# Performance work log

Hardware: AMD Instinct MI355X
Metric: run time of the kernel (lower is better)

Reference implementation:

```python
import jax, jax.numpy as jnp
import numpy as np

EMBED_DIM = 1024
NUM_HEADS = 16
HEAD_DIM = EMBED_DIM // NUM_HEADS
SCALE = float(np.sqrt(HEAD_DIM))


def setup_inputs() -> dict:
    key = jax.random.key(0)
    ks = jax.random.split(key, 5)
    B, S, D = 4, 2048, EMBED_DIM
    lim_qkv = 1.0 / np.sqrt(D)
    lim_out = 1.0 / np.sqrt(D)
    return {
        "x": jax.random.normal(ks[0], (B, S, D), dtype=jnp.float32),
        "qkv_w": jax.random.uniform(ks[1], (3 * D, D), jnp.float32, -lim_qkv, lim_qkv),
        "qkv_b": jax.random.uniform(ks[2], (3 * D,), jnp.float32, -lim_qkv, lim_qkv),
        "out_w": jax.random.uniform(ks[3], (D, D), jnp.float32, -lim_out, lim_out),
        "out_b": jax.random.uniform(ks[4], (D,), jnp.float32, -lim_out, lim_out),
    }


def reference(x, qkv_w, qkv_b, out_w, out_b):
    B, S, D = x.shape
    H, Hd = NUM_HEADS, HEAD_DIM
    # qkv projection (torch Linear: x @ W.T + b)
    qkv = x @ qkv_w.T + qkv_b                      # [B, S, 3D]
    qkv = qkv.reshape(B, S, 3, H, Hd)
    q = jnp.transpose(qkv[:, :, 0], (0, 2, 1, 3))  # [B, H, S, Hd]
    k = jnp.transpose(qkv[:, :, 1], (0, 2, 1, 3))
    v = jnp.transpose(qkv[:, :, 2], (0, 2, 1, 3))
    attn = jnp.einsum("bhqd,bhkd->bhqk", q, k) / SCALE  # [B, H, S, S]
    attn = jax.nn.softmax(attn, axis=-1)
    out = jnp.einsum("bhqk,bhkd->bhqd", attn, v)        # [B, H, S, Hd]
    out = jnp.transpose(out, (0, 2, 1, 3)).reshape(B, S, D)
    return out @ out_w.T + out_b
```

## Files before the change

### kernel.cpp

```cpp
#include <hip/hip_runtime.h>

typedef unsigned short u16;
typedef __bf16 bf16x8 __attribute__((ext_vector_type(8)));
typedef __bf16 bf16x4 __attribute__((ext_vector_type(4)));
typedef float f32x4 __attribute__((ext_vector_type(4)));
typedef float f32x16 __attribute__((ext_vector_type(16)));
typedef unsigned u32x2 __attribute__((ext_vector_type(2)));

#define AS1 __attribute__((address_space(1)))
#define AS3 __attribute__((address_space(3)))

__device__ __forceinline__ void gload_lds16(const void* g, void* l) {
  __builtin_amdgcn_global_load_lds((const AS1 void*)g, (AS3 void*)l, 16, 0, 0);
}

__device__ __forceinline__ f32x4 mfma16(bf16x8 a, bf16x8 b, f32x4 c) {
  return __builtin_amdgcn_mfma_f32_16x16x32_bf16(a, b, c, 0, 0, 0);
}
__device__ __forceinline__ f32x16 mfma32(bf16x8 a, bf16x8 b, f32x16 c) {
  return __builtin_amdgcn_mfma_f32_32x32x16_bf16(a, b, c, 0, 0, 0);
}

#define QSCALE 0.18033688011112042f

__global__ __launch_bounds__(256) void k_cvt3(const float* __restrict__ s0, u16* __restrict__ d0, int n0,
                                              const float* __restrict__ s1, u16* __restrict__ d1, int n1,
                                              const float* __restrict__ s2, u16* __restrict__ d2, int n2) {
  int g = (blockIdx.x * 256 + threadIdx.x) * 8;
  const float* src;
  u16* dst;
  int i;
  if (g < n0) { src = s0; dst = d0; i = g; }
  else if (g < n0 + n1) { src = s1; dst = d1; i = g - n0; }
  else if (g < n0 + n1 + n2) { src = s2; dst = d2; i = g - n0 - n1; }
  else return;
  float4 a = *(const float4*)(src + i);
  float4 b = *(const float4*)(src + i + 4);
  union { bf16x8 v; uint4 q; } o;
  o.v[0] = (__bf16)a.x; o.v[1] = (__bf16)a.y; o.v[2] = (__bf16)a.z; o.v[3] = (__bf16)a.w;
  o.v[4] = (__bf16)b.x; o.v[5] = (__bf16)b.y; o.v[6] = (__bf16)b.z; o.v[7] = (__bf16)b.w;
  *(uint4*)(dst + i) = o.q;
}

__global__ __launch_bounds__(512, 2) void k_gemm_qkv(
    const u16* __restrict__ A, const u16* __restrict__ W,
    const float* __restrict__ bias,
    u16* __restrict__ Qo, u16* __restrict__ Ko, u16* __restrict__ Vo) {
  __shared__ __align__(16) u16 LDS[2][6 * 4096];

  const int t = threadIdx.x;
  const int lane = t & 63;
  const int w = t >> 6;
  const int wm = w >> 1;
  const int wn = w & 1;
  const int lr = lane & 15;
  const int hi = lane >> 4;

  const int flat = blockIdx.x;
  const int nb = (flat & 7) * 96 + (flat >> 3);
  const int by = nb / 24;
  const int bx = nb - by * 24;
  const int m0 = by * 256;
  const int n0 = bx * 128;

  const int tt = t & 255;
  const int g = t >> 8;
  const int tu = (tt & 15) ^ (tt >> 4);
  const int sro = (tu >> 3) * 32 + (tt >> 4);
  const int scol = (tu & 7) * 8;

  auto STAGE = [&](int buf, int kt) {
#pragma unroll
    for (int p = 0; p < 3; ++p) {
      int st = p * 2 + g;
      const u16* base = (st < 4) ? (A + (size_t)(m0 + st * 64) * 1024)
                                 : (W + (size_t)(n0 + (st - 4) * 64) * 1024);
#pragma unroll
      for (int i = 0; i < 2; ++i)
        gload_lds16(base + (size_t)(sro + i * 16) * 1024 + kt * 64 + scol,
                    &LDS[buf][st * 4096 + i * 2048 + tt * 8]);
    }
  };

  f32x4 acc[4][4] = {};

  STAGE(0, 0);

  for (int kt = 0; kt < 16; ++kt) {
    const int cur = kt & 1;
    asm volatile("s_waitcnt vmcnt(0)" ::: "memory");
    __builtin_amdgcn_sched_barrier(0);
    __builtin_amdgcn_s_barrier();
    __builtin_amdgcn_sched_barrier(0);

    if (kt + 1 < 16) STAGE(cur ^ 1, kt + 1);

    const u16* ab = &LDS[cur][wm * 4096];
    const u16* bb = &LDS[cur][(4 + wn) * 4096];

    bf16x8 af[4][2], bfr[4][2];
#pragma unroll
    for (int mi = 0; mi < 4; ++mi)
#pragma unroll
      for (int ks = 0; ks < 2; ++ks)
        af[mi][ks] = *(const bf16x8*)(ab + ((mi & 1) * 16 + lr) * 128 +
                                      (((ks * 4 + hi + 8 * (mi >> 1)) ^ lr) << 3));
#pragma unroll
    for (int ni = 0; ni < 4; ++ni)
#pragma unroll
      for (int ks = 0; ks < 2; ++ks)
        bfr[ni][ks] = *(const bf16x8*)(bb + ((ni & 1) * 16 + lr) * 128 +
                                       (((ks * 4 + hi + 8 * (ni >> 1)) ^ lr) << 3));

    __builtin_amdgcn_s_setprio(1);
#pragma unroll
    for (int mi = 0; mi < 4; ++mi)
#pragma unroll
      for (int ni = 0; ni < 4; ++ni)
#pragma unroll
        for (int ks = 0; ks < 2; ++ks)
          acc[mi][ni] = mfma16(bfr[ni][ks], af[mi][ks], acc[mi][ni]);
    __builtin_amdgcn_s_setprio(0);
  }

  const int bb16 = m0 >> 11;
  const int sb = (m0 & 2047) + wm * 64;
  const int which = n0 >> 10;
  const int h = ((n0 & 1023) >> 6) + wn;
  float4 bv[4];
#pragma unroll
  for (int ni = 0; ni < 4; ++ni)
    bv[ni] = *(const float4*)(bias + n0 + wn * 64 + ni * 16 + hi * 4);

  if (which < 2) {
    const float scl = (which == 0) ? QSCALE : 1.0f;
    u16* dst = ((which == 0) ? Qo : Ko) + ((size_t)(bb16 * 16 + h) * 2048) * 64;
#pragma unroll
    for (int mi = 0; mi < 4; ++mi) {
      const int s = sb + mi * 16 + lr;
#pragma unroll
      for (int ni = 0; ni < 4; ++ni) {
        bf16x4 pk;
#pragma unroll
        for (int j = 0; j < 4; ++j)
          pk[j] = (__bf16)((acc[mi][ni][j] + ((const float*)&bv[ni])[j]) * scl);
        *(bf16x4*)(dst + (size_t)s * 64 + ni * 16 + hi * 4) = pk;
      }
    }
  } else {
    __syncthreads();
    u16* scr = &LDS[0][0] + w * 4608;
#pragma unroll
    for (int mi = 0; mi < 4; ++mi)
#pragma unroll
      for (int ni = 0; ni < 4; ++ni)
#pragma unroll
        for (int j = 0; j < 4; ++j) {
          union { __bf16 b; u16 u; } cv;
          cv.b = (__bf16)(acc[mi][ni][j] + ((const float*)&bv[ni])[j]);
          scr[(ni * 16 + hi * 4 + j) * 72 + mi * 16 + lr] = cv.u;
        }
    asm volatile("s_waitcnt lgkmcnt(0)" ::: "memory");
    __builtin_amdgcn_sched_barrier(0);
    u16* dst = Vo + ((size_t)((bb16 * 16 + h) * 64 + lane)) * 2048 + sb;
#pragma unroll
    for (int mc = 0; mc < 8; ++mc) {
      bf16x8 vv = *(const bf16x8*)(scr + lane * 72 + mc * 8);
      *(bf16x8*)(dst + mc * 8) = vv;
    }
  }
}

__global__ __launch_bounds__(256) void k_gemm_out(
    const u16* __restrict__ A, const u16* __restrict__ W,
    const float* __restrict__ bias, float* __restrict__ Cout,
    int M, int N, int K) {
  __shared__ __align__(16) u16 As[128 * 64];
  __shared__ __align__(16) u16 Bs[128 * 64];
  const int t = threadIdx.x;
  const int m0 = blockIdx.y * 128;
  const int n0 = blockIdx.x * 128;
  const int lane = t & 63;
  const int w = t >> 6;
  const int lr = lane & 15;
  const int hi = lane >> 4;
  const int wm = (w >> 1) * 64;
  const int wn = (w & 1) * 64;

  f32x4 acc[4][4] = {};

  const u16* aptr = A + (size_t)(m0 + (t >> 3)) * K + (t & 7) * 8;
  const u16* wptr = W + (size_t)(n0 + (t >> 3)) * K + (t & 7) * 8;

  for (int kt = 0; kt < K; kt += 64) {
#pragma unroll
    for (int i = 0; i < 4; i++)
      gload_lds16(aptr + (size_t)i * 32 * K + kt, As + i * 2048 + t * 8);
#pragma unroll
    for (int i = 0; i < 4; i++)
      gload_lds16(wptr + (size_t)i * 32 * K + kt, Bs + i * 2048 + t * 8);
    __syncthreads();
#pragma unroll
    for (int kk = 0; kk < 64; kk += 32) {
      bf16x8 af[4], bfr[4];
#pragma unroll
      for (int mi = 0; mi < 4; mi++)
        af[mi] = *(const bf16x8*)(As + (wm + mi * 16 + lr) * 64 + kk + hi * 8);
#pragma unroll
      for (int ni = 0; ni < 4; ni++)
        bfr[ni] = *(const bf16x8*)(Bs + (wn + ni * 16 + lr) * 64 + kk + hi * 8);
#pragma unroll
      for (int mi = 0; mi < 4; mi++)
#pragma unroll
        for (int ni = 0; ni < 4; ni++)
          acc[mi][ni] = mfma16(af[mi], bfr[ni], acc[mi][ni]);
    }
    __syncthreads();
  }

  float bv[4];
#pragma unroll
  for (int ni = 0; ni < 4; ni++) bv[ni] = bias[n0 + wn + ni * 16 + lr];

#pragma unroll
  for (int mi = 0; mi < 4; mi++)
#pragma unroll
    for (int j = 0; j < 4; j++) {
      int m = m0 + wm + mi * 16 + hi * 4 + j;
#pragma unroll
      for (int ni = 0; ni < 4; ni++)
        Cout[(size_t)m * N + n0 + wn + ni * 16 + lr] = acc[mi][ni][j] + bv[ni];
    }
}

__global__ __launch_bounds__(256, 4) void k_attn(const u16* __restrict__ Q,
                                                 const u16* __restrict__ K,
                                                 const u16* __restrict__ Vt,
                                                 u16* __restrict__ ctx) {
  __shared__ __align__(16) u16 Ks[2][64 * 64];
  __shared__ __align__(16) u16 Vs[2][64 * 64];

  const int t = threadIdx.x;
  const int lane = t & 63;
  const int w = t >> 6;
  const int r31 = lane & 31;
  const int hw = lane >> 5;

  const int bid = blockIdx.x;
  const int nb = (bid & 7) * 128 + (bid >> 3);
  const int bh = nb >> 4;
  const int q0 = (nb & 15) * 128;

  const u16* qp = Q + (size_t)bh * 2048 * 64;
  const u16* kp = K + (size_t)bh * 2048 * 64;
  const u16* vp = Vt + (size_t)bh * 64 * 2048;

  const int tu = (t & 15) ^ (t >> 4);
  const int srow = (tu >> 3) * 32 + (t >> 4);
  const int scol = (tu & 7) * 8;

#pragma unroll
  for (int i = 0; i < 2; i++)
    gload_lds16(kp + (size_t)(srow + i * 16) * 64 + scol, Ks[0] + i * 2048 + t * 8);
#pragma unroll
  for (int i = 0; i < 2; i++)
    gload_lds16(vp + (size_t)(srow + i * 16) * 2048 + scol, Vs[0] + i * 2048 + t * 8);

  bf16x8 aq[4];
  const u16* qrow = qp + (size_t)(q0 + w * 32 + r31) * 64 + hw * 8;
#pragma unroll
  for (int kd = 0; kd < 4; kd++) aq[kd] = *(const bf16x8*)(qrow + kd * 16);

  bf16x8 ones;
#pragma unroll
  for (int e = 0; e < 8; e++) ones[e] = (__bf16)1.0f;

  asm volatile("s_waitcnt vmcnt(0)" ::: "memory");
  __builtin_amdgcn_sched_barrier(0);
  __builtin_amdgcn_s_barrier();
  __builtin_amdgcn_sched_barrier(0);

  f32x16 o0 = {}, o1 = {}, l_acc = {};

  for (int kt = 0; kt < 32; kt++) {
    const int cur = kt & 1;
    if (kt + 1 < 32) {
      u16* kd_ = Ks[cur ^ 1];
      u16* vd_ = Vs[cur ^ 1];
#pragma unroll
      for (int i = 0; i < 2; i++)
        gload_lds16(kp + (size_t)((kt + 1) * 64 + srow + i * 16) * 64 + scol,
                    kd_ + i * 2048 + t * 8);
#pragma unroll
      for (int i = 0; i < 2; i++)
        gload_lds16(vp + (size_t)(srow + i * 16) * 2048 + (kt + 1) * 64 + scol,
                    vd_ + i * 2048 + t * 8);
      asm volatile("s_waitcnt vmcnt(4)" ::: "memory");
    } else {
      asm volatile("s_waitcnt vmcnt(0)" ::: "memory");
    }
    __builtin_amdgcn_sched_barrier(0);
    __builtin_amdgcn_s_barrier();
    __builtin_amdgcn_sched_barrier(0);

    const u16* kb = Ks[cur];
    const u16* vb = Vs[cur];

    f32x16 s0 = {}, s1 = {};
    __builtin_amdgcn_s_setprio(1);
#pragma unroll
    for (int kd = 0; kd < 4; kd++) {
      int sl0 = (((kd * 2 + hw) ^ (r31 & 15)) << 3);
      int sl1 = (((8 + kd * 2 + hw) ^ (r31 & 15)) << 3);
      bf16x8 ka0 = *(const bf16x8*)(kb + r31 * 128 + sl0);
      bf16x8 ka1 = *(const bf16x8*)(kb + r31 * 128 + sl1);
      s0 = mfma32(ka0, aq[kd], s0);
      s1 = mfma32(ka1, aq[kd], s1);
    }
    __builtin_amdgcn_s_setprio(0);

#pragma unroll
    for (int e = 0; e < 16; e++) {
      s0[e] = __builtin_amdgcn_exp2f(s0[e]);
      s1[e] = __builtin_amdgcn_exp2f(s1[e]);
    }

    __builtin_amdgcn_s_setprio(1);
#pragma unroll
    for (int tile = 0; tile < 2; tile++) {
      f32x16 st = tile ? s1 : s0;
      unsigned pk[8];
#pragma unroll
      for (int p = 0; p < 8; p++) {
        union { __bf16 h[2]; unsigned u; } cv;
        cv.h[0] = (__bf16)st[2 * p];
        cv.h[1] = (__bf16)st[2 * p + 1];
        pk[p] = cv.u;
      }
#pragma unroll
      for (int c = 0; c < 2; c++) {
        u32x2 ra = __builtin_amdgcn_permlane32_swap(pk[4 * c], pk[4 * c + 2], false, false);
        u32x2 rb = __builtin_amdgcn_permlane32_swap(pk[4 * c + 1], pk[4 * c + 3], false, false);
        union { unsigned u[4]; bf16x8 v; } pf;
        pf.u[0] = ra[0]; pf.u[1] = rb[0]; pf.u[2] = ra[1]; pf.u[3] = rb[1];
        const int kap = tile * 2 + c;
        int slv0 = (((kap * 2 + hw) ^ (r31 & 15)) << 3);
        int slv1 = (((8 + kap * 2 + hw) ^ (r31 & 15)) << 3);
        bf16x8 v0 = *(const bf16x8*)(vb + r31 * 128 + slv0);
        bf16x8 v1 = *(const bf16x8*)(vb + r31 * 128 + slv1);
        o0 = mfma32(v0, pf.v, o0);
        o1 = mfma32(v1, pf.v, o1);
        l_acc = mfma32(ones, pf.v, l_acc);
      }
    }
    __builtin_amdgcn_s_setprio(0);
    __builtin_amdgcn_sched_barrier(0);
    __builtin_amdgcn_s_barrier();
  }

  const int bb = bh >> 4, h = bh & 15;
  const float inv = 1.0f / l_acc[0];
  const size_t base = (size_t)(bb * 2048 + q0 + w * 32 + r31) * 1024 + h * 64;
#pragma unroll
  for (int g = 0; g < 4; g++) {
    bf16x4 p0, p1;
#pragma unroll
    for (int j = 0; j < 4; j++) {
      p0[j] = (__bf16)(o0[g * 4 + j] * inv);
      p1[j] = (__bf16)(o1[g * 4 + j] * inv);
    }
    *(bf16x4*)(ctx + base + g * 8 + hw * 4) = p0;
    *(bf16x4*)(ctx + base + 32 + g * 8 + hw * 4) = p1;
  }
}

extern "C" void kernel_launch(void* const* d_in, const int* in_sizes, int n_in,
                              void* d_out, int out_size, void* d_ws, size_t ws_size,
                              hipStream_t stream) {
  const float* x = (const float*)d_in[0];
  const float* qkv_w = (const float*)d_in[1];
  const float* qkv_b = (const float*)d_in[2];
  const float* out_w = (const float*)d_in[3];
  const float* out_b = (const float*)d_in[4];
  float* out = (float*)d_out;
  char* ws = (char*)d_ws;

  u16* xb    = (u16*)(ws + 0);
  u16* wqkvb = (u16*)(ws + 16777216);
  u16* wob   = (u16*)(ws + 23068672);
  u16* Qb    = (u16*)(ws + 25165824);
  u16* Kb    = (u16*)(ws + 41943040);
  u16* Vtb   = (u16*)(ws + 58720256);
  u16* ctx   = xb;

  k_cvt3<<<6144, 256, 0, stream>>>(x, xb, 8388608,
                                   qkv_w, wqkvb, 3145728,
                                   out_w, wob, 1048576);

  k_gemm_qkv<<<768, 512, 0, stream>>>(xb, wqkvb, qkv_b, Qb, Kb, Vtb);
  k_attn<<<1024, 256, 0, stream>>>(Qb, Kb, Vtb, ctx);
  k_gemm_out<<<dim3(8, 64), 256, 0, stream>>>(ctx, wob, out_b, out,
                                              8192, 1024, 1024);
}
```

Measured before the change: 204.3 us.

## Template QKV GEMM for reuse as output GEMM and interleave staging with MFMA

The pipelined, swizzled 256x128 GEMM kernel becomes a template used for both the QKV projection and the output projection, replacing the simpler, unpipelined 128x128 out-projection GEMM. The main loop now splits each K tile into two halves: half of the next tile's global-to-LDS staging is issued per half, with an extra barrier between halves, so loads overlap MFMA work more evenly and fewer fragments sit in registers. The output GEMM now runs only 256 blocks, which may leave some compute units underused, and the extra barrier adds synchronisation cost.

```diff
diff --git a/kernel.cpp b/kernel.cpp
--- a/kernel.cpp
+++ b/kernel.cpp
@@ -42,9 +42,10 @@
   *(uint4*)(dst + i) = o.q;
 }
 
-__global__ __launch_bounds__(512, 2) void k_gemm_qkv(
+template <int MODE, int BXN>
+__global__ __launch_bounds__(512, 2) void k_gemm_big(
     const u16* __restrict__ A, const u16* __restrict__ W,
-    const float* __restrict__ bias,
+    const float* __restrict__ bias, float* __restrict__ Cout,
     u16* __restrict__ Qo, u16* __restrict__ Ko, u16* __restrict__ Vo) {
   __shared__ __align__(16) u16 LDS[2][6 * 4096];
 
@@ -56,10 +57,11 @@
   const int lr = lane & 15;
   const int hi = lane >> 4;
 
+  const int TOT = BXN * 32;
   const int flat = blockIdx.x;
-  const int nb = (flat & 7) * 96 + (flat >> 3);
-  const int by = nb / 24;
-  const int bx = nb - by * 24;
+  const int nb = (flat & 7) * (TOT >> 3) + (flat >> 3);
+  const int by = nb / BXN;
+  const int bx = nb - by * BXN;
   const int m0 = by * 256;
   const int n0 = bx * 128;
 
@@ -69,9 +71,8 @@
   const int sro = (tu >> 3) * 32 + (tt >> 4);
   const int scol = (tu & 7) * 8;
 
-  auto STAGE = [&](int buf, int kt) {
-#pragma unroll
-    for (int p = 0; p < 3; ++p) {
+  auto STAGE = [&](int buf, int kt, int pLo, int pHi) {
+    for (int p = pLo; p < pHi; ++p) {
       int st = p * 2 + g;
       const u16* base = (st < 4) ? (A + (size_t)(m0 + st * 64) * 1024)
                                  : (W + (size_t)(n0 + (st - 4) * 64) * 1024);
@@ -84,7 +85,7 @@
 
   f32x4 acc[4][4] = {};
 
-  STAGE(0, 0);
+  STAGE(0, 0, 0, 3);
 
   for (int kt = 0; kt < 16; ++kt) {
     const int cur = kt & 1;
@@ -93,144 +94,95 @@
     __builtin_amdgcn_s_barrier();
     __builtin_amdgcn_sched_barrier(0);
 
-    if (kt + 1 < 16) STAGE(cur ^ 1, kt + 1);
-
     const u16* ab = &LDS[cur][wm * 4096];
     const u16* bb = &LDS[cur][(4 + wn) * 4096];
 
-    bf16x8 af[4][2], bfr[4][2];
-#pragma unroll
-    for (int mi = 0; mi < 4; ++mi)
-#pragma unroll
-      for (int ks = 0; ks < 2; ++ks)
-        af[mi][ks] = *(const bf16x8*)(ab + ((mi & 1) * 16 + lr) * 128 +
-                                      (((ks * 4 + hi + 8 * (mi >> 1)) ^ lr) << 3));
-#pragma unroll
-    for (int ni = 0; ni < 4; ++ni)
-#pragma unroll
-      for (int ks = 0; ks < 2; ++ks)
-        bfr[ni][ks] = *(const bf16x8*)(bb + ((ni & 1) * 16 + lr) * 128 +
-                                       (((ks * 4 + hi + 8 * (ni >> 1)) ^ lr) << 3));
-
-    __builtin_amdgcn_s_setprio(1);
-#pragma unroll
-    for (int mi = 0; mi < 4; ++mi)
+#pragma unroll
+    for (int ks = 0; ks < 2; ++ks) {
+      bf16x8 af[4], bfr[4];
+#pragma unroll
+      for (int mi = 0; mi < 4; ++mi)
+        af[mi] = *(const bf16x8*)(ab + ((mi & 1) * 16 + lr) * 128 +
+                                  (((ks * 4 + hi + 8 * (mi >> 1)) ^ lr) << 3));
 #pragma unroll
       for (int ni = 0; ni < 4; ++ni)
-#pragma unroll
-        for (int ks = 0; ks < 2; ++ks)
-          acc[mi][ni] = mfma16(bfr[ni][ks], af[mi][ks], acc[mi][ni]);
-    __builtin_amdgcn_s_setprio(0);
+        bfr[ni] = *(const bf16x8*)(bb + ((ni & 1) * 16 + lr) * 128 +
+                                   (((ks * 4 + hi + 8 * (ni >> 1)) ^ lr) << 3));
+      if (kt + 1 < 16) STAGE(cur ^ 1, kt + 1, ks ? 2 : 0, ks ? 3 : 2);
+      asm volatile("s_waitcnt lgkmcnt(0)" ::: "memory");
+      __builtin_amdgcn_sched_barrier(0);
+      __builtin_amdgcn_s_setprio(1);
+#pragma unroll
+      for (int mi = 0; mi < 4; ++mi)
+#pragma unroll
+        for (int ni = 0; ni < 4; ++ni)
+          acc[mi][ni] = mfma16(bfr[ni], af[mi], acc[mi][ni]);
+      __builtin_amdgcn_s_setprio(0);
+      __builtin_amdgcn_sched_barrier(0);
+      if (ks == 0) __builtin_amdgcn_s_barrier();
+    }
   }
 
-  const int bb16 = m0 >> 11;
-  const int sb = (m0 & 2047) + wm * 64;
-  const int which = n0 >> 10;
-  const int h = ((n0 & 1023) >> 6) + wn;
-  float4 bv[4];
+  f32x4 bv[4];
 #pragma unroll
   for (int ni = 0; ni < 4; ++ni)
-    bv[ni] = *(const float4*)(bias + n0 + wn * 64 + ni * 16 + hi * 4);
-
-  if (which < 2) {
-    const float scl = (which == 0) ? QSCALE : 1.0f;
-    u16* dst = ((which == 0) ? Qo : Ko) + ((size_t)(bb16 * 16 + h) * 2048) * 64;
+    bv[ni] = *(const f32x4*)(bias + n0 + wn * 64 + ni * 16 + hi * 4);
+
+  if (MODE == 0) {
+    const int N = BXN * 128;
 #pragma unroll
     for (int mi = 0; mi < 4; ++mi) {
-      const int s = sb + mi * 16 + lr;
+      const int m = m0 + wm * 64 + mi * 16 + lr;
 #pragma unroll
       for (int ni = 0; ni < 4; ++ni) {
-        bf16x4 pk;
-#pragma unroll
-        for (int j = 0; j < 4; ++j)
-          pk[j] = (__bf16)((acc[mi][ni][j] + ((const float*)&bv[ni])[j]) * scl);
-        *(bf16x4*)(dst + (size_t)s * 64 + ni * 16 + hi * 4) = pk;
+        f32x4 o = acc[mi][ni] + bv[ni];
+        *(f32x4*)(Cout + (size_t)m * N + n0 + wn * 64 + ni * 16 + hi * 4) = o;
       }
     }
   } else {
-    __syncthreads();
-    u16* scr = &LDS[0][0] + w * 4608;
-#pragma unroll
-    for (int mi = 0; mi < 4; ++mi)
-#pragma unroll
-      for (int ni = 0; ni < 4; ++ni)
-#pragma unroll
-        for (int j = 0; j < 4; ++j) {
-          union { __bf16 b; u16 u; } cv;
-          cv.b = (__bf16)(acc[mi][ni][j] + ((const float*)&bv[ni])[j]);
-          scr[(ni * 16 + hi * 4 + j) * 72 + mi * 16 + lr] = cv.u;
+    const int bb16 = m0 >> 11;
+    const int sb = (m0 & 2047) + wm * 64;
+    const int which = n0 >> 10;
+    const int h = ((n0 & 1023) >> 6) + wn;
+
+    if (which < 2) {
+      const float scl = (which == 0) ? QSCALE : 1.0f;
+      u16* dst = ((which == 0) ? Qo : Ko) + ((size_t)(bb16 * 16 + h) * 2048) * 64;
+#pragma unroll
+      for (int mi = 0; mi < 4; ++mi) {
+        const int s = sb + mi * 16 + lr;
+#pragma unroll
+        for (int ni = 0; ni < 4; ++ni) {
+          bf16x4 pk;
+#pragma unroll
+          for (int j = 0; j < 4; ++j)
+            pk[j] = (__bf16)((acc[mi][ni][j] + bv[ni][j]) * scl);
+          *(bf16x4*)(dst + (size_t)s * 64 + ni * 16 + hi * 4) = pk;
         }
-    asm volatile("s_waitcnt lgkmcnt(0)" ::: "memory");
-    __builtin_amdgcn_sched_barrier(0);
-    u16* dst = Vo + ((size_t)((bb16 * 16 + h) * 64 + lane)) * 2048 + sb;
-#pragma unroll
-    for (int mc = 0; mc < 8; ++mc) {
-      bf16x8 vv = *(const bf16x8*)(scr + lane * 72 + mc * 8);
-      *(bf16x8*)(dst + mc * 8) = vv;
+      }
+    } else {
+      __syncthreads();
+      u16* scr = &LDS[0][0] + w * 4608;
+#pragma unroll
+      for (int mi = 0; mi < 4; ++mi)
+#pragma unroll
+        for (int ni = 0; ni < 4; ++ni)
+#pragma unroll
+          for (int j = 0; j < 4; ++j) {
+            union { __bf16 b; u16 u; } cv;
+            cv.b = (__bf16)(acc[mi][ni][j] + bv[ni][j]);
+            scr[(ni * 16 + hi * 4 + j) * 72 + mi * 16 + lr] = cv.u;
+          }
+      asm volatile("s_waitcnt lgkmcnt(0)" ::: "memory");
+      __builtin_amdgcn_sched_barrier(0);
+      u16* dst = Vo + ((size_t)((bb16 * 16 + h) * 64 + lane)) * 2048 + sb;
+#pragma unroll
+      for (int mc = 0; mc < 8; ++mc) {
+        bf16x8 vv = *(const bf16x8*)(scr + lane * 72 + mc * 8);
+        *(bf16x8*)(dst + mc * 8) = vv;
+      }
     }
   }
-}
-
-__global__ __launch_bounds__(256) void k_gemm_out(
-    const u16* __restrict__ A, const u16* __restrict__ W,
-    const float* __restrict__ bias, float* __restrict__ Cout,
-    int M, int N, int K) {
-  __shared__ __align__(16) u16 As[128 * 64];
-  __shared__ __align__(16) u16 Bs[128 * 64];
-  const int t = threadIdx.x;
-  const int m0 = blockIdx.y * 128;
-  const int n0 = blockIdx.x * 128;
-  const int lane = t & 63;
-  const int w = t >> 6;
-  const int lr = lane & 15;
-  const int hi = lane >> 4;
-  const int wm = (w >> 1) * 64;
-  const int wn = (w & 1) * 64;
-
-  f32x4 acc[4][4] = {};
-
-  const u16* aptr = A + (size_t)(m0 + (t >> 3)) * K + (t & 7) * 8;
-  const u16* wptr = W + (size_t)(n0 + (t >> 3)) * K + (t & 7) * 8;
-
-  for (int kt = 0; kt < K; kt += 64) {
-#pragma unroll
-    for (int i = 0; i < 4; i++)
-      gload_lds16(aptr + (size_t)i * 32 * K + kt, As + i * 2048 + t * 8);
-#pragma unroll
-    for (int i = 0; i < 4; i++)
-      gload_lds16(wptr + (size_t)i * 32 * K + kt, Bs + i * 2048 + t * 8);
-    __syncthreads();
-#pragma unroll
-    for (int kk = 0; kk < 64; kk += 32) {
-      bf16x8 af[4], bfr[4];
-#pragma unroll
-      for (int mi = 0; mi < 4; mi++)
-        af[mi] = *(const bf16x8*)(As + (wm + mi * 16 + lr) * 64 + kk + hi * 8);
-#pragma unroll
-      for (int ni = 0; ni < 4; ni++)
-        bfr[ni] = *(const bf16x8*)(Bs + (wn + ni * 16 + lr) * 64 + kk + hi * 8);
-#pragma unroll
-      for (int mi = 0; mi < 4; mi++)
-#pragma unroll
-        for (int ni = 0; ni < 4; ni++)
-          acc[mi][ni] = mfma16(af[mi], bfr[ni], acc[mi][ni]);
-    }
-    __syncthreads();
-  }
-
-  float bv[4];
-#pragma unroll
-  for (int ni = 0; ni < 4; ni++) bv[ni] = bias[n0 + wn + ni * 16 + lr];
-
-#pragma unroll
-  for (int mi = 0; mi < 4; mi++)
-#pragma unroll
-    for (int j = 0; j < 4; j++) {
-      int m = m0 + wm + mi * 16 + hi * 4 + j;
-#pragma unroll
-      for (int ni = 0; ni < 4; ni++)
-        Cout[(size_t)m * N + n0 + wn + ni * 16 + lr] = acc[mi][ni][j] + bv[ni];
-    }
 }
 
 __global__ __launch_bounds__(256, 4) void k_attn(const u16* __restrict__ Q,
@@ -397,8 +349,9 @@
                                    qkv_w, wqkvb, 3145728,
                                    out_w, wob, 1048576);
 
-  k_gemm_qkv<<<768, 512, 0, stream>>>(xb, wqkvb, qkv_b, Qb, Kb, Vtb);
+  k_gemm_big<1, 24><<<768, 512, 0, stream>>>(xb, wqkvb, qkv_b, nullptr,
+                                             Qb, Kb, Vtb);
   k_attn<<<1024, 256, 0, stream>>>(Qb, Kb, Vtb, ctx);
-  k_gemm_out<<<dim3(8, 64), 256, 0, stream>>>(ctx, wob, out_b, out,
-                                              8192, 1024, 1024);
-}
+  k_gemm_big<0, 8><<<256, 512, 0, stream>>>(ctx, wob, out_b, out,
+                                            nullptr, nullptr, nullptr);
+}
```

Result: faster. 198.6 us (-2.8%).
